# Kernel optimization log

Hardware: AMD Instinct MI355X
Metric: run time of the kernel (lower is better)

The kernel has to match this reference:

```python
import jax, jax.numpy as jnp
import numpy as np
import math

D_MODEL = 512
EXPAND = 1
D_INNER = EXPAND * D_MODEL          # 512
HALF = D_INNER // 2                 # 256 per-branch channels
D_STATE = D_MODEL // 4 * EXPAND     # 128 (overrides d_state arg in __init__)
DT_RANK = math.ceil(D_MODEL / 16)   # 32
D_CONV = 4


def _dwconv_same(x, w):
    # x: (B, C, L), w: (C, 1, k); torch padding='same' for k=4 -> pad (left=1, right=2)
    k = w.shape[-1]
    total = k - 1
    left = total // 2
    return jax.lax.conv_general_dilated(
        x, w, window_strides=(1,), padding=[(left, total - left)],
        feature_group_count=w.shape[0], dimension_numbers=("NCH", "OIH", "NCH"))


def _sparse_approx(m):
    thr = jnp.max(m) * 0.1
    return jnp.sign(m) * jax.nn.relu(jnp.abs(m) - thr)


def _selective_scan(u, delta, A, Bc, Cc, D):
    # u, delta: (B, d, L); A: (d, n); Bc, Cc: (B, n, L); D: (d,)
    dT = jnp.moveaxis(delta, 2, 0)   # (L, B, d)
    uT = jnp.moveaxis(u, 2, 0)       # (L, B, d)
    BT = jnp.moveaxis(Bc, 2, 0)      # (L, B, n)
    CT = jnp.moveaxis(Cc, 2, 0)      # (L, B, n)

    def step(h, inputs):
        d_t, u_t, b_t, c_t = inputs                      # (B,d),(B,d),(B,n),(B,n)
        dA = jnp.exp(d_t[..., None] * A)                 # (B, d, n)
        dBu = d_t[..., None] * b_t[:, None, :] * u_t[..., None]
        h = dA * h + dBu                                 # (B, d, n)
        y = jnp.einsum("bdn,bn->bd", h, c_t)
        return h, y

    h0 = jnp.zeros((u.shape[0], u.shape[1], A.shape[1]), dtype=u.dtype)
    _, ys = jax.lax.scan(step, h0, (dT, uT, BT, CT))     # ys: (L, B, d)
    y = jnp.moveaxis(ys, 0, 2)                           # (B, d, L)
    return y + u * D[:, None]


def _branch(inph, in_w, cx_w, cz_w, xproj_w, dt_w, dt_b, out_w, A, D):
    # inph: (B, L, d_model)
    xz = jnp.swapaxes(inph @ in_w.T, 1, 2)   # (B, d_inner, L)
    x, z = xz[:, :HALF], xz[:, HALF:]
    x = jax.nn.silu(_dwconv_same(x, cx_w))   # (B, half, L); conv bias is False (True//2==0)
    z = jax.nn.silu(_dwconv_same(z, cz_w))
    x_dbl = jnp.swapaxes(x, 1, 2) @ xproj_w.T        # (B, L, dt_rank + 2n)
    dt = x_dbl[..., :DT_RANK] @ dt_w.T               # (B, L, half)
    dt = jnp.swapaxes(dt, 1, 2)                      # (B, half, L)
    Bc = jnp.swapaxes(x_dbl[..., DT_RANK:DT_RANK + D_STATE], 1, 2)   # (B, n, L)
    Cc = jnp.swapaxes(x_dbl[..., DT_RANK + D_STATE:], 1, 2)          # (B, n, L)
    Bc = _sparse_approx(Bc)
    Cc = _sparse_approx(Cc)
    delta = jax.nn.softplus(dt + dt_b[None, :, None])
    y = _selective_scan(x, delta, A, Bc, Cc, D)
    out = jnp.concatenate([y, z], axis=1)            # (B, d_inner, L)
    return jnp.swapaxes(out, 1, 2) @ out_w.T         # (B, L, d_model)


def setup_inputs() -> dict:
    key = jax.random.key(0)
    ks = jax.random.split(key, 16)
    B, L = 2, 2048
    s = lambda fan: 1.0 / np.sqrt(fan)

    inp = jax.random.normal(ks[0], (B, 2 * D_MODEL, L), jnp.float32)

    in_proj_w = jax.random.uniform(ks[1], (D_INNER, D_MODEL), jnp.float32, -s(D_MODEL), s(D_MODEL))
    x_proj_w = jax.random.uniform(ks[2], (DT_RANK + 2 * D_STATE, HALF), jnp.float32, -s(HALF), s(HALF))
    dt_init_std = DT_RANK ** (-0.5)
    dt_proj_w = jax.random.uniform(ks[3], (HALF, DT_RANK), jnp.float32, -dt_init_std, dt_init_std)
    out_proj_w = jax.random.uniform(ks[4], (D_MODEL, D_INNER), jnp.float32, -s(D_INNER), s(D_INNER))

    in_proj_2_w = jax.random.uniform(ks[5], (D_INNER, D_MODEL), jnp.float32, -s(D_MODEL), s(D_MODEL))
    x_proj_2_w = jax.random.uniform(ks[6], (DT_RANK + 2 * D_STATE, HALF), jnp.float32, -s(HALF), s(HALF))
    dt_proj_2_w = jax.random.uniform(ks[7], (HALF, DT_RANK), jnp.float32, -dt_init_std, dt_init_std)
    out_proj_2_w = jax.random.uniform(ks[8], (D_MODEL, D_INNER), jnp.float32, -s(D_INNER), s(D_INNER))

    # dt bias init: inverse-softplus of dt ~ LogUniform(1e-3, 1e-1), floor 1e-4
    def inv_softplus_dt(k):
        u = jax.random.uniform(k, (HALF,), jnp.float32)
        dt = jnp.exp(u * (np.log(0.1) - np.log(0.001)) + np.log(0.001))
        dt = jnp.clip(dt, 1e-4, None)
        return dt + jnp.log(-jnp.expm1(-dt))
    dt_proj_b = inv_softplus_dt(ks[9])
    dt_proj_2_b = inv_softplus_dt(ks[10])

    cs = 1.0 / np.sqrt(D_CONV)  # depthwise conv fan_in = 1*k
    conv_x_w = jax.random.uniform(ks[11], (HALF, 1, D_CONV), jnp.float32, -cs, cs)
    conv_z_w = jax.random.uniform(ks[12], (HALF, 1, D_CONV), jnp.float32, -cs, cs)
    conv_x_2_w = jax.random.uniform(ks[13], (HALF, 1, D_CONV), jnp.float32, -cs, cs)
    conv_z_2_w = jax.random.uniform(ks[14], (HALF, 1, D_CONV), jnp.float32, -cs, cs)

    A_log = jnp.log(jnp.broadcast_to(jnp.arange(1, D_STATE + 1, dtype=jnp.float32), (HALF, D_STATE)))
    D = jnp.ones((HALF,), jnp.float32)
    epsilon = jnp.array([0.01], jnp.float32)

    return dict(inp=inp, in_proj_w=in_proj_w, conv_x_w=conv_x_w, conv_z_w=conv_z_w,
                x_proj_w=x_proj_w, dt_proj_w=dt_proj_w, dt_proj_b=dt_proj_b, out_proj_w=out_proj_w,
                in_proj_2_w=in_proj_2_w, conv_x_2_w=conv_x_2_w, conv_z_2_w=conv_z_2_w,
                x_proj_2_w=x_proj_2_w, dt_proj_2_w=dt_proj_2_w, dt_proj_2_b=dt_proj_2_b,
                out_proj_2_w=out_proj_2_w, A_log=A_log, D=D, epsilon=epsilon)


def reference(inp, in_proj_w, conv_x_w, conv_z_w, x_proj_w, dt_proj_w, dt_proj_b, out_proj_w,
              in_proj_2_w, conv_x_2_w, conv_z_2_w, x_proj_2_w, dt_proj_2_w, dt_proj_2_b,
              out_proj_2_w, A_log, D, epsilon):
    # inp: (B, 2*d_model, L) -> split along dim 1, permute to (B, L, d_model)
    inpx = jnp.swapaxes(inp[:, :D_MODEL, :], 1, 2)
    inpy = jnp.swapaxes(inp[:, D_MODEL:, :], 1, 2)

    A_base = (1.0 + epsilon[0]) * (-jnp.exp(A_log))
    A1 = _sparse_approx(A_base)        # branch 1
    A2 = _sparse_approx(A1)            # branch 2 sparsifies the already-sparsified A

    out1 = _branch(inpx, in_proj_w, conv_x_w, conv_z_w, x_proj_w, dt_proj_w, dt_proj_b, out_proj_w, A1, D)
    out2 = _branch(inpy, in_proj_2_w, conv_x_2_w, conv_z_2_w, x_proj_2_w, dt_proj_2_w, dt_proj_2_b, out_proj_2_w, A2, D)
    return out1, out2
```

## Files before the change

kernel.cpp:

```cpp
#include <hip/hip_runtime.h>
#include <math.h>

constexpr int B_    = 2;
constexpr int L_    = 2048;
constexpr int NROW  = B_ * L_;
constexpr int MROW  = 2 * NROW;
constexpr int HALF_ = 256;
constexpr int DS_   = 128;

constexpr float LOG2E = 1.4426950408889634f;

constexpr size_t OFF_MINP = 0;
constexpr size_t OFF_BCMX = 32;
constexpr size_t OFF_XZ   = 64;
constexpr size_t OFF_YT   = OFF_XZ + (size_t)MROW * 256;
constexpr size_t OFF_XDBL = OFF_XZ + (size_t)MROW * 512;
constexpr size_t OFF_XS   = OFF_XDBL + (size_t)MROW * 288;
constexpr size_t OFF_BS   = OFF_XS  + (size_t)MROW * 256;
constexpr size_t OFF_CS   = OFF_BS  + (size_t)2 * NROW * 128;
constexpr size_t OFF_DTT  = OFF_CS  + (size_t)2 * NROW * 128;
constexpr size_t OFF_DUT  = OFF_DTT + (size_t)2 * 256 * 4096;
constexpr size_t OFF_UDT  = OFF_DUT + (size_t)2 * 256 * 4096;
constexpr size_t FLOAT_END = OFF_UDT + (size_t)2 * 256 * 4096;

constexpr size_t HOFF_XINH = 0;
constexpr size_t HOFF_XINL = HOFF_XINH + (size_t)MROW * 512;
constexpr size_t HOFF_YZH  = HOFF_XINH;
constexpr size_t HOFF_YZL  = HOFF_XINL;
constexpr size_t HOFF_XSH  = HOFF_XINL + (size_t)MROW * 512;
constexpr size_t HOFF_XSL  = HOFF_XSH  + (size_t)MROW * 256;
constexpr size_t HOFF_INWH = HOFF_XSL  + (size_t)MROW * 256;
constexpr size_t HOFF_INWL = HOFF_INWH + 524288;
constexpr size_t HOFF_XWH  = HOFF_INWL + 524288;
constexpr size_t HOFF_XWL  = HOFF_XWH  + 147456;
constexpr size_t HOFF_OUTWH= HOFF_XWL  + 147456;
constexpr size_t HOFF_OUTWL= HOFF_OUTWH+ 524288;

constexpr size_t WST_IN = 262144;
constexpr size_t WST_X  = 73728;

constexpr int PRE_MINA = 32;
constexpr int PRE_WSPL = (1196032 + 255) / 256;
constexpr int PRE_TIN  = 64 * 16 * 4;
constexpr int PRE_BLOCKS = PRE_MINA + PRE_WSPL + PRE_TIN;

typedef __bf16 bf16x8 __attribute__((ext_vector_type(8)));
typedef float  f32x4  __attribute__((ext_vector_type(4)));

__device__ __forceinline__ unsigned short bf16rn(float x) {
    unsigned u = __float_as_uint(x);
    unsigned r = (u + 0x7FFFu + ((u >> 16) & 1u)) >> 16;
    return (unsigned short)r;
}
__device__ __forceinline__ void split2(float x, unsigned short& h, unsigned short& l) {
    h = bf16rn(x);
    float hf = __uint_as_float(((unsigned)h) << 16);
    l = bf16rn(x - hf);
}

__device__ __forceinline__ float shrinkf(float v, float thr) {
    float a = fabsf(v) - thr;
    a = fmaxf(a, 0.0f);
    float r = copysignf(a, v);
    return (v == 0.0f) ? 0.0f : r;
}
__device__ __forceinline__ float siluf(float v) { return v / (1.0f + __expf(-v)); }
__device__ __forceinline__ float softplusf(float v) {
    return fmaxf(v, 0.0f) + log1pf(__expf(-fabsf(v)));
}
__device__ __forceinline__ float rlanef(float v, int l) {
    return __int_as_float(__builtin_amdgcn_readlane(__float_as_int(v), l));
}
__device__ __forceinline__ unsigned fkey(float f) {
    unsigned u = __float_as_uint(f);
    return (u >> 31) ? ~u : (u | 0x80000000u);
}
__device__ __forceinline__ float funkey(unsigned k) {
    unsigned u = (k >> 31) ? (k & 0x7FFFFFFFu) : ~k;
    return __uint_as_float(u);
}

__global__ __launch_bounds__(256) void pre_all(const float* __restrict__ A_log,
                                               const float* __restrict__ inp,
                                               const float* __restrict__ in_w0,
                                               const float* __restrict__ in_w1,
                                               const float* __restrict__ outw0,
                                               const float* __restrict__ outw1,
                                               const float* __restrict__ xw0,
                                               const float* __restrict__ xw1,
                                               float* __restrict__ ws,
                                               unsigned* __restrict__ bcmax,
                                               unsigned short* __restrict__ hb) {
    int bid = blockIdx.x;
    int tid = threadIdx.x;
    if (bid < PRE_MINA) {
        __shared__ float sbuf[8];
        int i = bid * 1024 + tid * 4;
        float4 v = *(const float4*)(A_log + i);
        float mv = fminf(fminf(v.x, v.y), fminf(v.z, v.w));
        #pragma unroll
        for (int off = 32; off > 0; off >>= 1) mv = fminf(mv, __shfl_xor(mv, off));
        if ((tid & 63) == 0) sbuf[tid >> 6] = mv;
        __syncthreads();
        if (tid == 0) {
            float r = fminf(fminf(sbuf[0], sbuf[1]), fminf(sbuf[2], sbuf[3]));
            ws[OFF_MINP + bid] = r;
        }
        if (bid == 0 && tid < 4) bcmax[tid] = 0u;
    } else if (bid < PRE_MINA + PRE_WSPL) {
        int i = (bid - PRE_MINA) * 256 + tid;
        if (i >= 1196032) return;
        const float* src;
        size_t hbase, lbase;
        int off;
        if (i < 1048576) {
            int t = i >> 18;
            off = i & 262143;
            src = (t == 0) ? in_w0 : (t == 1) ? in_w1 : (t == 2) ? outw0 : outw1;
            if (t < 2) { hbase = HOFF_INWH + (size_t)t * WST_IN;  lbase = HOFF_INWL + (size_t)t * WST_IN; }
            else       { hbase = HOFF_OUTWH + (size_t)(t - 2) * WST_IN; lbase = HOFF_OUTWL + (size_t)(t - 2) * WST_IN; }
        } else {
            int j = i - 1048576;
            int t = (j < (int)WST_X) ? 0 : 1;
            off = j - t * (int)WST_X;
            src = t ? xw1 : xw0;
            hbase = HOFF_XWH + (size_t)t * WST_X;
            lbase = HOFF_XWL + (size_t)t * WST_X;
        }
        unsigned short h, l;
        split2(src[off], h, l);
        hb[hbase + off] = h;
        hb[lbase + off] = l;
    } else {
        __shared__ float tile[32][33];
        int idx = bid - PRE_MINA - PRE_WSPL;
        int bx = idx & 63;
        int by = (idx >> 6) & 15;
        int z  = idx >> 10;
        int br = z >> 1;
        int b  = z & 1;
        int t0 = bx * 32;
        int m0 = by * 32;
        int tx = tid & 31;
        int ty = tid >> 5;
        #pragma unroll
        for (int k = 0; k < 4; k++) {
            tile[ty + 8 * k][tx] =
                inp[((size_t)b * 1024 + br * 512 + m0 + ty + 8 * k) * L_ + t0 + tx];
        }
        __syncthreads();
        #pragma unroll
        for (int k = 0; k < 4; k++) {
            size_t dst = ((size_t)br * NROW + (size_t)b * L_ + t0 + ty + 8 * k) * 512 + m0 + tx;
            unsigned short h, l;
            split2(tile[tx][ty + 8 * k], h, l);
            hb[HOFF_XINH + dst] = h;
            hb[HOFF_XINL + dst] = l;
        }
    }
}

template <int NGUARD, int DOMAX>
__global__ __launch_bounds__(256) void gemm_mfma(const unsigned short* __restrict__ Ah,
                                                 const unsigned short* __restrict__ Al, int lda,
                                                 const unsigned short* __restrict__ WhB,
                                                 const unsigned short* __restrict__ WlB,
                                                 size_t wstride,
                                                 float* __restrict__ C, int ldc,
                                                 int N, int K,
                                                 unsigned* __restrict__ bcmax) {
    __shared__ __align__(16) unsigned short sAh[128 * 40];
    __shared__ __align__(16) unsigned short sAl[128 * 40];
    __shared__ __align__(16) unsigned short sBh[64 * 40];
    __shared__ __align__(16) unsigned short sBl[64 * 40];
    int tid  = threadIdx.x;
    int wid  = tid >> 6;
    int lane = tid & 63;
    int fr   = lane & 15;
    int kg   = lane >> 4;
    int mblk = blockIdx.y * 128;
    int nblk = blockIdx.x * 64;
    int br   = (mblk >= NROW) ? 1 : 0;
    const unsigned short* Wh = WhB + (size_t)br * wstride;
    const unsigned short* Wl = WlB + (size_t)br * wstride;
    int srow = tid >> 2;
    int skp  = (tid & 3) * 8;
    bool brow_ok = (!NGUARD) || ((nblk + srow) < N);

    const unsigned short* pA0 = Ah + (size_t)(mblk + srow) * lda + skp;
    const unsigned short* pA1 = Ah + (size_t)(mblk + 64 + srow) * lda + skp;
    const unsigned short* pL0 = Al + (size_t)(mblk + srow) * lda + skp;
    const unsigned short* pL1 = Al + (size_t)(mblk + 64 + srow) * lda + skp;
    const unsigned short* pBh = Wh + (size_t)(nblk + srow) * K + skp;
    const unsigned short* pBl = Wl + (size_t)(nblk + srow) * K + skp;

    f32x4 acc[2][4] = {};

    uint4 rah0 = *(const uint4*)(pA0);
    uint4 rah1 = *(const uint4*)(pA1);
    uint4 ral0 = *(const uint4*)(pL0);
    uint4 ral1 = *(const uint4*)(pL1);
    uint4 rbh = {0, 0, 0, 0}, rbl = {0, 0, 0, 0};
    if (brow_ok) {
        rbh = *(const uint4*)(pBh);
        rbl = *(const uint4*)(pBl);
    }

    for (int k0 = 0; k0 < K; k0 += 32) {
        __syncthreads();
        *(uint4*)(sAh + srow * 40 + skp) = rah0;
        *(uint4*)(sAh + (64 + srow) * 40 + skp) = rah1;
        *(uint4*)(sAl + srow * 40 + skp) = ral0;
        *(uint4*)(sAl + (64 + srow) * 40 + skp) = ral1;
        *(uint4*)(sBh + srow * 40 + skp) = rbh;
        *(uint4*)(sBl + srow * 40 + skp) = rbl;
        __syncthreads();

        int kn = k0 + 32;
        if (kn < K) {
            rah0 = *(const uint4*)(pA0 + kn);
            rah1 = *(const uint4*)(pA1 + kn);
            ral0 = *(const uint4*)(pL0 + kn);
            ral1 = *(const uint4*)(pL1 + kn);
            if (brow_ok) {
                rbh = *(const uint4*)(pBh + kn);
                rbl = *(const uint4*)(pBl + kn);
            }
        }

        bf16x8 ah0 = *(const bf16x8*)(sAh + (wid * 32 + fr) * 40 + kg * 8);
        bf16x8 ah1 = *(const bf16x8*)(sAh + (wid * 32 + 16 + fr) * 40 + kg * 8);
        bf16x8 al0 = *(const bf16x8*)(sAl + (wid * 32 + fr) * 40 + kg * 8);
        bf16x8 al1 = *(const bf16x8*)(sAl + (wid * 32 + 16 + fr) * 40 + kg * 8);
        #pragma unroll
        for (int nt = 0; nt < 4; nt++) {
            bf16x8 bh = *(const bf16x8*)(sBh + (nt * 16 + fr) * 40 + kg * 8);
            bf16x8 bl = *(const bf16x8*)(sBl + (nt * 16 + fr) * 40 + kg * 8);
            acc[0][nt] = __builtin_amdgcn_mfma_f32_16x16x32_bf16(ah0, bh, acc[0][nt], 0, 0, 0);
            acc[0][nt] = __builtin_amdgcn_mfma_f32_16x16x32_bf16(ah0, bl, acc[0][nt], 0, 0, 0);
            acc[0][nt] = __builtin_amdgcn_mfma_f32_16x16x32_bf16(al0, bh, acc[0][nt], 0, 0, 0);
            acc[1][nt] = __builtin_amdgcn_mfma_f32_16x16x32_bf16(ah1, bh, acc[1][nt], 0, 0, 0);
            acc[1][nt] = __builtin_amdgcn_mfma_f32_16x16x32_bf16(ah1, bl, acc[1][nt], 0, 0, 0);
            acc[1][nt] = __builtin_amdgcn_mfma_f32_16x16x32_bf16(al1, bh, acc[1][nt], 0, 0, 0);
        }
    }
    #pragma unroll
    for (int mt = 0; mt < 2; mt++) {
        #pragma unroll
        for (int nt = 0; nt < 4; nt++) {
            int col = nblk + nt * 16 + fr;
            if (NGUARD && col >= N) continue;
            #pragma unroll
            for (int r = 0; r < 4; r++) {
                int row = mblk + wid * 32 + mt * 16 + kg * 4 + r;
                C[(size_t)row * ldc + col] = acc[mt][nt][r];
            }
        }
    }
    if (DOMAX) {
        float mb = -INFINITY, mc = -INFINITY;
        #pragma unroll
        for (int nt = 0; nt < 4; nt++) {
            int c16 = nblk + nt * 16;
            if (c16 >= 32 && c16 < 160) {
                #pragma unroll
                for (int mt = 0; mt < 2; mt++)
                    #pragma unroll
                    for (int r = 0; r < 4; r++) mb = fmaxf(mb, acc[mt][nt][r]);
            } else if (c16 >= 160 && c16 < 288) {
                #pragma unroll
                for (int mt = 0; mt < 2; mt++)
                    #pragma unroll
                    for (int r = 0; r < 4; r++) mc = fmaxf(mc, acc[mt][nt][r]);
            }
        }
        #pragma unroll
        for (int off = 32; off > 0; off >>= 1) {
            mb = fmaxf(mb, __shfl_xor(mb, off));
            mc = fmaxf(mc, __shfl_xor(mc, off));
        }
        if (lane == 0) {
            if (mb > -INFINITY) atomicMax(bcmax + 2 * br,     fkey(mb));
            if (mc > -INFINITY) atomicMax(bcmax + 2 * br + 1, fkey(mc));
        }
    }
}

__global__ __launch_bounds__(256) void conv_silu_kernel(const float* __restrict__ xz,
                                                        float* __restrict__ xs,
                                                        unsigned short* __restrict__ xsh,
                                                        unsigned short* __restrict__ xsl,
                                                        unsigned short* __restrict__ yzh,
                                                        unsigned short* __restrict__ yzl,
                                                        const float* __restrict__ wx0,
                                                        const float* __restrict__ wx1,
                                                        const float* __restrict__ wz0,
                                                        const float* __restrict__ wz1) {
    int gid = blockIdx.x * 256 + threadIdx.x;
    int c4  = (gid & 63) << 2;
    int row = gid >> 6;
    int br  = row >> 12;
    int t   = row & (L_ - 1);
    const float* wx = br ? wx1 : wx0;
    const float* wz = br ? wz1 : wz0;
    float4 wxv[4], wzv[4];
    #pragma unroll
    for (int k = 0; k < 4; k++) {
        wxv[k] = *(const float4*)(wx + (c4 + k) * 4);
        wzv[k] = *(const float4*)(wz + (c4 + k) * 4);
    }
    float4 ax = {0, 0, 0, 0}, az = {0, 0, 0, 0};
    #pragma unroll
    for (int j = 0; j < 4; j++) {
        int tt = t + j - 1;
        if (tt >= 0 && tt < L_) {
            const float* p = xz + (size_t)(row + j - 1) * 512;
            float4 vx = *(const float4*)(p + c4);
            float4 vz = *(const float4*)(p + 256 + c4);
            ax.x = fmaf(vx.x, ((const float*)&wxv[0])[j], ax.x);
            ax.y = fmaf(vx.y, ((const float*)&wxv[1])[j], ax.y);
            ax.z = fmaf(vx.z, ((const float*)&wxv[2])[j], ax.z);
            ax.w = fmaf(vx.w, ((const float*)&wxv[3])[j], ax.w);
            az.x = fmaf(vz.x, ((const float*)&wzv[0])[j], az.x);
            az.y = fmaf(vz.y, ((const float*)&wzv[1])[j], az.y);
            az.z = fmaf(vz.z, ((const float*)&wzv[2])[j], az.z);
            az.w = fmaf(vz.w, ((const float*)&wzv[3])[j], az.w);
        }
    }
    float4 sx, sz;
    sx.x = siluf(ax.x); sx.y = siluf(ax.y); sx.z = siluf(ax.z); sx.w = siluf(ax.w);
    sz.x = siluf(az.x); sz.y = siluf(az.y); sz.z = siluf(az.z); sz.w = siluf(az.w);
    *(float4*)(xs + (size_t)row * 256 + c4) = sx;
    ushort4 hx, lx, hz, lz;
    split2(sx.x, hx.x, lx.x); split2(sx.y, hx.y, lx.y);
    split2(sx.z, hx.z, lx.z); split2(sx.w, hx.w, lx.w);
    split2(sz.x, hz.x, lz.x); split2(sz.y, hz.y, lz.y);
    split2(sz.z, hz.z, lz.z); split2(sz.w, hz.w, lz.w);
    *(ushort4*)(xsh + (size_t)row * 256 + c4) = hx;
    *(ushort4*)(xsl + (size_t)row * 256 + c4) = lx;
    *(ushort4*)(yzh + (size_t)row * 512 + 256 + c4) = hz;
    *(ushort4*)(yzl + (size_t)row * 512 + 256 + c4) = lz;
}

__global__ __launch_bounds__(256) void dtprep_shrink(const float* __restrict__ A, int lda,
                                                     const float* __restrict__ W0,
                                                     const float* __restrict__ W1,
                                                     const float* __restrict__ b0,
                                                     const float* __restrict__ b1,
                                                     const float* __restrict__ xs,
                                                     const float* __restrict__ Dvec,
                                                     float* __restrict__ dtT,
                                                     float* __restrict__ duT,
                                                     float* __restrict__ udT,
                                                     const unsigned* __restrict__ bcmax,
                                                     float* __restrict__ Bs,
                                                     float* __restrict__ Cs) {
    __shared__ float As[16][68];
    __shared__ float Ws[16][68];
    __shared__ float tb[64 * 68];
    int tid = threadIdx.x;
    int kk = tid & 15;
    int rr = tid >> 4;
    int mblk = blockIdx.y * 64;
    int nblk = blockIdx.x * 64;
    int br = (mblk >= NROW) ? 1 : 0;
    const float* W    = br ? W1 : W0;
    const float* bias = br ? b1 : b0;
    float acc[4][4] = {};
    for (int k0 = 0; k0 < 32; k0 += 16) {
        #pragma unroll
        for (int j = 0; j < 4; j++) {
            As[kk][rr + 16 * j] = A[(size_t)(mblk + rr + 16 * j) * lda + k0 + kk];
        }
        #pragma unroll
        for (int j = 0; j < 4; j++) {
            Ws[kk][rr + 16 * j] = W[(size_t)(nblk + rr + 16 * j) * 32 + k0 + kk];
        }
        __syncthreads();
        int ty = tid >> 4;
        int tx = tid & 15;
        #pragma unroll
        for (int kq = 0; kq < 16; kq++) {
            float a0 = As[kq][ty * 4 + 0];
            float a1 = As[kq][ty * 4 + 1];
            float a2 = As[kq][ty * 4 + 2];
            float a3 = As[kq][ty * 4 + 3];
            float v0 = Ws[kq][tx * 4 + 0];
            float v1 = Ws[kq][tx * 4 + 1];
            float v2 = Ws[kq][tx * 4 + 2];
            float v3 = Ws[kq][tx * 4 + 3];
            acc[0][0] = fmaf(a0, v0, acc[0][0]); acc[0][1] = fmaf(a0, v1, acc[0][1]);
            acc[0][2] = fmaf(a0, v2, acc[0][2]); acc[0][3] = fmaf(a0, v3, acc[0][3]);
            acc[1][0] = fmaf(a1, v0, acc[1][0]); acc[1][1] = fmaf(a1, v1, acc[1][1]);
            acc[1][2] = fmaf(a1, v2, acc[1][2]); acc[1][3] = fmaf(a1, v3, acc[1][3]);
            acc[2][0] = fmaf(a2, v0, acc[2][0]); acc[2][1] = fmaf(a2, v1, acc[2][1]);
            acc[2][2] = fmaf(a2, v2, acc[2][2]); acc[2][3] = fmaf(a2, v3, acc[2][3]);
            acc[3][0] = fmaf(a3, v0, acc[3][0]); acc[3][1] = fmaf(a3, v1, acc[3][1]);
            acc[3][2] = fmaf(a3, v2, acc[3][2]); acc[3][3] = fmaf(a3, v3, acc[3][3]);
        }
        __syncthreads();
    }
    int ty = tid >> 4;
    int tx = tid & 15;
    float dlt[4][4], uu[4][4];
    #pragma unroll
    for (int i = 0; i < 4; i++) {
        int m = mblk + ty * 4 + i;
        #pragma unroll
        for (int j = 0; j < 4; j++) {
            int n = nblk + tx * 4 + j;
            dlt[i][j] = softplusf(acc[i][j] + bias[n]);
            uu[i][j]  = xs[(size_t)m * 256 + n];
        }
    }
    float Dv[4];
    #pragma unroll
    for (int j = 0; j < 4; j++) Dv[j] = Dvec[nblk + tx * 4 + j];

    int mlocbase = mblk & (NROW - 1);
    int nrd  = tid >> 2;
    int mc   = (tid & 3) * 4;
    size_t obase = ((size_t)br * 256 + nblk + nrd) * 4096 + mlocbase;
    #pragma unroll
    for (int pass = 0; pass < 3; pass++) {
        __syncthreads();
        #pragma unroll
        for (int i = 0; i < 4; i++) {
            #pragma unroll
            for (int j = 0; j < 4; j++) {
                float v = (pass == 0) ? dlt[i][j] * LOG2E
                        : (pass == 1) ? dlt[i][j] * uu[i][j]
                                      : uu[i][j] * Dv[j];
                tb[(tx * 4 + j) * 68 + ty * 4 + i] = v;
            }
        }
        __syncthreads();
        float* dst = (pass == 0) ? dtT : (pass == 1) ? duT : udT;
        #pragma unroll
        for (int it = 0; it < 4; it++) {
            int cc = mc + it * 16;
            float4 v = *(const float4*)(tb + nrd * 68 + cc);
            *(float4*)(dst + obase + cc) = v;
        }
    }
    {
        int q = blockIdx.x;
        int isC = q >> 1;
        int cbase = (q & 1) * 64;
        int xoff = isC ? (160 + cbase) : (32 + cbase);
        float thr = 0.1f * funkey(bcmax[2 * br + isC]);
        float* dstArr = isC ? Cs : Bs;
        int r = tid >> 2;
        int c0 = (tid & 3) * 16;
        const float* src = A + (size_t)(mblk + r) * lda + xoff + c0;
        float* dp = dstArr + (size_t)(mblk + r) * 128 + cbase + c0;
        #pragma unroll
        for (int i = 0; i < 16; i += 4) {
            float4 v = *(const float4*)(src + i);
            float4 o;
            o.x = shrinkf(v.x, thr);
            o.y = shrinkf(v.y, thr);
            o.z = shrinkf(v.z, thr);
            o.w = shrinkf(v.w, thr);
            *(float4*)(dp + i) = o;
        }
    }
}

__global__ __launch_bounds__(128) void scan10_kernel(float* __restrict__ ws,
                                                     const float* __restrict__ A_log,
                                                     const float* __restrict__ eps) {
    int blk  = blockIdx.x;
    int xcd  = blk & 7;
    int slot = blk >> 3;
    int combo = xcd >> 1;
    int d  = (xcd & 1) * 128 + slot;
    int br = combo >> 1;
    int b  = combo & 1;
    int tid = threadIdx.x;
    int lt  = tid & 63;
    int half = tid >> 6;

    float pv = ws[OFF_MINP + (tid & 31)];
    #pragma unroll
    for (int off = 16; off > 0; off >>= 1) pv = fminf(pv, __shfl_xor(pv, off));
    float e  = 1.0f + eps[0];
    float m1 = -e * __expf(pv);
    float t1 = 0.1f * m1;
    float t2 = 0.1f * shrinkf(m1, t1);
    float base = -e * __expf(A_log[d * 128 + tid]);
    float a = shrinkf(base, t1);
    if (br) a = shrinkf(a, t2);

    size_t dchain = ((size_t)br * 256 + d) * 4096 + (size_t)b * L_;
    const float* dtp = ws + OFF_DTT + dchain;
    const float* dup = ws + OFF_DUT + dchain;
    const float* udp = ws + OFF_UDT + dchain;
    const float* Bq  = ws + OFF_BS + ((size_t)br * NROW + (size_t)b * L_) * 128 + tid;
    const float* Cq  = ws + OFF_CS + ((size_t)br * NROW + (size_t)b * L_) * 128 + tid;
    float*       yTp = ws + OFF_YT + dchain;

    __shared__ float red[64 * 132];
    __shared__ float comb[2][64];

    float h = 0.0f;

    float Bb[2][8], Cb[2][8];
    #pragma unroll
    for (int j = 0; j < 8; j++) { Bb[0][j] = Bq[j * 128]; Cb[0][j] = Cq[j * 128]; }
    Bq += 1024; Cq += 1024;
    #pragma unroll
    for (int j = 0; j < 8; j++) { Bb[1][j] = Bq[j * 128]; Cb[1][j] = Cq[j * 128]; }
    Bq += 1024; Cq += 1024;

    float dt_c = dtp[lt];
    float du_c = dup[lt];
    float dt_n = 0.0f, du_n = 0.0f;

    for (int c = 0; c < 32; c++) {
        if (c < 31) { dt_n = dtp[64 + lt]; du_n = dup[64 + lt]; }
        dtp += 64; dup += 64;
        float ud_c = udp[c * 64 + lt];
        #pragma unroll
        for (int m = 0; m < 8; m++) {
            const int cur = m & 1;
            #pragma unroll
            for (int j = 0; j < 8; j++) {
                const int tl = m * 8 + j;
                float dt2 = rlanef(dt_c, tl);
                float du  = rlanef(du_c, tl);
                float ev = __builtin_amdgcn_exp2f(dt2 * a);
                h = fmaf(ev, h, du * Bb[cur][j]);
                red[tl * 132 + half * 64 + lt] = h * Cb[cur][j];
            }
            #pragma unroll
            for (int j = 0; j < 8; j++) {
                Bb[cur][j] = Bq[j * 128];
                Cb[cur][j] = Cq[j * 128];
            }
            Bq += 1024; Cq += 1024;
        }
        __builtin_amdgcn_wave_barrier();
        {
            const float* rp = &red[lt * 132 + half * 64];
            float s0 = 0.f, s1 = 0.f, s2 = 0.f, s3 = 0.f;
            #pragma unroll
            for (int i = 0; i < 64; i += 4) {
                float4 v = *(const float4*)(rp + i);
                s0 += v.x; s1 += v.y; s2 += v.z; s3 += v.w;
            }
            float part = (s0 + s1) + (s2 + s3);
            if (half) comb[c & 1][lt] = part;
            __syncthreads();
            if (!half) yTp[c * 64 + lt] = part + comb[c & 1][lt] + ud_c;
        }
        __builtin_amdgcn_wave_barrier();
        dt_c = dt_n;
        du_c = du_n;
    }
}

__global__ __launch_bounds__(256) void transpose_yz_kernel(const float* __restrict__ yT,
                                                           unsigned short* __restrict__ yzh,
                                                           unsigned short* __restrict__ yzl) {
    __shared__ float tile[32][33];
    int br = blockIdx.z;
    int m0 = blockIdx.x * 32;
    int n0 = blockIdx.y * 32;
    int tx = threadIdx.x;
    int ty = threadIdx.y;
    #pragma unroll
    for (int k = 0; k < 4; k++) {
        tile[ty + 8 * k][tx] = yT[((size_t)br * 256 + m0 + ty + 8 * k) * 4096 + n0 + tx];
    }
    __syncthreads();
    #pragma unroll
    for (int k = 0; k < 4; k++) {
        size_t dst = ((size_t)br * NROW + n0 + ty + 8 * k) * 512 + m0 + tx;
        unsigned short h, l;
        split2(tile[tx][ty + 8 * k], h, l);
        yzh[dst] = h; yzl[dst] = l;
    }
}

extern "C" void kernel_launch(void* const* d_in, const int* in_sizes, int n_in,
                              void* d_out, int out_size, void* d_ws, size_t ws_size,
                              hipStream_t stream) {
    const float* inp   = (const float*)d_in[0];
    const float* in_w[2]  = {(const float*)d_in[1],  (const float*)d_in[8]};
    const float* cxw[2]   = {(const float*)d_in[2],  (const float*)d_in[9]};
    const float* czw[2]   = {(const float*)d_in[3],  (const float*)d_in[10]};
    const float* xw[2]    = {(const float*)d_in[4],  (const float*)d_in[11]};
    const float* dtw[2]   = {(const float*)d_in[5],  (const float*)d_in[12]};
    const float* dtb[2]   = {(const float*)d_in[6],  (const float*)d_in[13]};
    const float* outw[2]  = {(const float*)d_in[7],  (const float*)d_in[14]};
    const float* A_log = (const float*)d_in[15];
    const float* Dvec  = (const float*)d_in[16];
    const float* eps   = (const float*)d_in[17];
    float* out = (float*)d_out;
    float* ws  = (float*)d_ws;
    unsigned short* hb = (unsigned short*)(ws + FLOAT_END);
    unsigned* bcmax = (unsigned*)(ws + OFF_BCMX);

    pre_all<<<PRE_BLOCKS, 256, 0, stream>>>(
        A_log, inp, in_w[0], in_w[1], outw[0], outw[1], xw[0], xw[1],
        ws, bcmax, hb);

    gemm_mfma<0, 0><<<dim3(512 / 64, MROW / 128), 256, 0, stream>>>(
        hb + HOFF_XINH, hb + HOFF_XINL, 512,
        hb + HOFF_INWH, hb + HOFF_INWL, WST_IN,
        ws + OFF_XZ, 512, 512, 512, nullptr);

    conv_silu_kernel<<<(MROW * 64) / 256, 256, 0, stream>>>(
        ws + OFF_XZ, ws + OFF_XS, hb + HOFF_XSH, hb + HOFF_XSL,
        hb + HOFF_YZH, hb + HOFF_YZL, cxw[0], cxw[1], czw[0], czw[1]);

    gemm_mfma<1, 1><<<dim3((288 + 63) / 64, MROW / 128), 256, 0, stream>>>(
        hb + HOFF_XSH, hb + HOFF_XSL, 256,
        hb + HOFF_XWH, hb + HOFF_XWL, WST_X,
        ws + OFF_XDBL, 288, 288, 256, bcmax);

    dtprep_shrink<<<dim3(4, MROW / 64), 256, 0, stream>>>(
        ws + OFF_XDBL, 288, dtw[0], dtw[1], dtb[0], dtb[1],
        ws + OFF_XS, Dvec,
        ws + OFF_DTT, ws + OFF_DUT, ws + OFF_UDT,
        bcmax, ws + OFF_BS, ws + OFF_CS);

    scan10_kernel<<<dim3(1024), 128, 0, stream>>>(ws, A_log, eps);

    transpose_yz_kernel<<<dim3(256 / 32, NROW / 32, 2), dim3(32, 8), 0, stream>>>(
        ws + OFF_YT, hb + HOFF_YZH, hb + HOFF_YZL);

    gemm_mfma<0, 0><<<dim3(512 / 64, MROW / 128), 256, 0, stream>>>(
        hb + HOFF_YZH, hb + HOFF_YZL, 512,
        hb + HOFF_OUTWH, hb + HOFF_OUTWL, WST_IN,
        out, 512, 512, 512, nullptr);
}
```

Baseline: 322.3 us.

## Split selective scan into two-pass chunked scan over sequence halves

The single sequential scan over 2048 timesteps is replaced by two kernels. The first runs the state recurrence over the first half only, without the C reduction, and stores the final hidden state. The second processes both sequence halves in parallel, seeding the second half with the stored state. This shortens the serial dependency chain and raises parallelism, in exchange for recomputing the first half's recurrence and an extra kernel launch.

```diff
diff --git a/kernel.cpp b/kernel.cpp
--- a/kernel.cpp
+++ b/kernel.cpp
@@ -13,6 +13,7 @@
 constexpr size_t OFF_MINP = 0;
 constexpr size_t OFF_BCMX = 32;
 constexpr size_t OFF_XZ   = 64;
+constexpr size_t OFF_HIN  = OFF_XZ;
 constexpr size_t OFF_YT   = OFF_XZ + (size_t)MROW * 256;
 constexpr size_t OFF_XDBL = OFF_XZ + (size_t)MROW * 512;
 constexpr size_t OFF_XS   = OFF_XDBL + (size_t)MROW * 288;
@@ -467,9 +468,9 @@
     }
 }
 
-__global__ __launch_bounds__(128) void scan10_kernel(float* __restrict__ ws,
-                                                     const float* __restrict__ A_log,
-                                                     const float* __restrict__ eps) {
+__global__ __launch_bounds__(128) void scan_pass1(float* __restrict__ ws,
+                                                  const float* __restrict__ A_log,
+                                                  const float* __restrict__ eps) {
     int blk  = blockIdx.x;
     int xcd  = blk & 7;
     int slot = blk >> 3;
@@ -479,7 +480,6 @@
     int b  = combo & 1;
     int tid = threadIdx.x;
     int lt  = tid & 63;
-    int half = tid >> 6;
 
     float pv = ws[OFF_MINP + (tid & 31)];
     #pragma unroll
@@ -495,32 +495,26 @@
     size_t dchain = ((size_t)br * 256 + d) * 4096 + (size_t)b * L_;
     const float* dtp = ws + OFF_DTT + dchain;
     const float* dup = ws + OFF_DUT + dchain;
-    const float* udp = ws + OFF_UDT + dchain;
     const float* Bq  = ws + OFF_BS + ((size_t)br * NROW + (size_t)b * L_) * 128 + tid;
     const float* Cq  = ws + OFF_CS + ((size_t)br * NROW + (size_t)b * L_) * 128 + tid;
-    float*       yTp = ws + OFF_YT + dchain;
-
-    __shared__ float red[64 * 132];
-    __shared__ float comb[2][64];
+    (void)Cq;
 
     float h = 0.0f;
-
-    float Bb[2][8], Cb[2][8];
-    #pragma unroll
-    for (int j = 0; j < 8; j++) { Bb[0][j] = Bq[j * 128]; Cb[0][j] = Cq[j * 128]; }
-    Bq += 1024; Cq += 1024;
-    #pragma unroll
-    for (int j = 0; j < 8; j++) { Bb[1][j] = Bq[j * 128]; Cb[1][j] = Cq[j * 128]; }
-    Bq += 1024; Cq += 1024;
+    float Bb[2][8];
+    #pragma unroll
+    for (int j = 0; j < 8; j++) Bb[0][j] = Bq[j * 128];
+    Bq += 1024;
+    #pragma unroll
+    for (int j = 0; j < 8; j++) Bb[1][j] = Bq[j * 128];
+    Bq += 1024;
 
     float dt_c = dtp[lt];
     float du_c = dup[lt];
     float dt_n = 0.0f, du_n = 0.0f;
 
-    for (int c = 0; c < 32; c++) {
-        if (c < 31) { dt_n = dtp[64 + lt]; du_n = dup[64 + lt]; }
+    for (int c = 0; c < 16; c++) {
+        if (c < 15) { dt_n = dtp[64 + lt]; du_n = dup[64 + lt]; }
         dtp += 64; dup += 64;
-        float ud_c = udp[c * 64 + lt];
         #pragma unroll
         for (int m = 0; m < 8; m++) {
             const int cur = m & 1;
@@ -531,30 +525,122 @@
                 float du  = rlanef(du_c, tl);
                 float ev = __builtin_amdgcn_exp2f(dt2 * a);
                 h = fmaf(ev, h, du * Bb[cur][j]);
-                red[tl * 132 + half * 64 + lt] = h * Cb[cur][j];
             }
             #pragma unroll
-            for (int j = 0; j < 8; j++) {
-                Bb[cur][j] = Bq[j * 128];
-                Cb[cur][j] = Cq[j * 128];
+            for (int j = 0; j < 8; j++) Bb[cur][j] = Bq[j * 128];
+            Bq += 1024;
+        }
+        dt_c = dt_n;
+        du_c = du_n;
+    }
+    ws[OFF_HIN + (((size_t)(br * 2 + b) * 256 + d) * 128 + tid)] = h;
+}
+
+__global__ __launch_bounds__(256) void scan_pass2(float* __restrict__ ws,
+                                                  const float* __restrict__ A_log,
+                                                  const float* __restrict__ eps) {
+    int blk  = blockIdx.x;
+    int xcd  = blk & 7;
+    int slot = blk >> 3;
+    int dhalf = xcd & 1;
+    int combo = xcd >> 1;
+    int br = combo >> 1;
+    int b  = combo & 1;
+    int chunk = slot >> 6;
+    int pairIdx = slot & 63;
+    int tid = threadIdx.x;
+    int ch  = tid >> 7;
+    int nid = tid & 127;
+    int lt  = tid & 63;
+    int half = (tid >> 6) & 1;
+    int d = dhalf * 128 + pairIdx * 2 + ch;
+
+    float pv = ws[OFF_MINP + (tid & 31)];
+    #pragma unroll
+    for (int off = 16; off > 0; off >>= 1) pv = fminf(pv, __shfl_xor(pv, off));
+    float e  = 1.0f + eps[0];
+    float m1 = -e * __expf(pv);
+    float t1 = 0.1f * m1;
+    float t2 = 0.1f * shrinkf(m1, t1);
+    float base = -e * __expf(A_log[d * 128 + nid]);
+    float a = shrinkf(base, t1);
+    if (br) a = shrinkf(a, t2);
+
+    size_t dchain = ((size_t)br * 256 + d) * 4096 + (size_t)b * L_;
+    size_t tb0 = (size_t)chunk * 1024;
+    const float* dtp = ws + OFF_DTT + dchain + tb0;
+    const float* dup = ws + OFF_DUT + dchain + tb0;
+    const float* udp = ws + OFF_UDT + dchain + tb0;
+    const float* Bq  = ws + OFF_BS + ((size_t)br * NROW + (size_t)b * L_ + tb0) * 128 + nid;
+    const float* Cq  = ws + OFF_CS + ((size_t)br * NROW + (size_t)b * L_ + tb0) * 128 + nid;
+    float*       yTp = ws + OFF_YT + dchain + tb0;
+
+    __shared__ float red[2][32 * 132];
+    __shared__ float comb[2][2][32];
+
+    float h = 0.0f;
+    if (chunk) h = ws[OFF_HIN + (((size_t)(br * 2 + b) * 256 + d) * 128 + nid)];
+
+    float Bb[2][8], Cb[2][8];
+    #pragma unroll
+    for (int j = 0; j < 8; j++) { Bb[0][j] = Bq[j * 128]; Cb[0][j] = Cq[j * 128]; }
+    Bq += 1024; Cq += 1024;
+    #pragma unroll
+    for (int j = 0; j < 8; j++) { Bb[1][j] = Bq[j * 128]; Cb[1][j] = Cq[j * 128]; }
+    Bq += 1024; Cq += 1024;
+
+    float dt_c = dtp[lt];
+    float du_c = dup[lt];
+    float dt_n = 0.0f, du_n = 0.0f;
+
+    int tp = lt >> 1;
+    int q  = lt & 1;
+
+    for (int cc = 0; cc < 16; cc++) {
+        if (cc < 15) { dt_n = dtp[64 + lt]; du_n = dup[64 + lt]; }
+        dtp += 64; dup += 64;
+        #pragma unroll
+        for (int g = 0; g < 2; g++) {
+            float ud_c = udp[cc * 64 + g * 32 + tp];
+            #pragma unroll
+            for (int m = 0; m < 4; m++) {
+                const int cur = m & 1;
+                #pragma unroll
+                for (int j = 0; j < 8; j++) {
+                    const int tl = g * 32 + m * 8 + j;
+                    const int tloc = m * 8 + j;
+                    float dt2 = rlanef(dt_c, tl);
+                    float du  = rlanef(du_c, tl);
+                    float ev = __builtin_amdgcn_exp2f(dt2 * a);
+                    h = fmaf(ev, h, du * Bb[cur][j]);
+                    red[ch][tloc * 132 + half * 64 + lt] = h * Cb[cur][j];
+                }
+                #pragma unroll
+                for (int j = 0; j < 8; j++) {
+                    Bb[cur][j] = Bq[j * 128];
+                    Cb[cur][j] = Cq[j * 128];
+                }
+                Bq += 1024; Cq += 1024;
             }
-            Bq += 1024; Cq += 1024;
-        }
-        __builtin_amdgcn_wave_barrier();
-        {
-            const float* rp = &red[lt * 132 + half * 64];
-            float s0 = 0.f, s1 = 0.f, s2 = 0.f, s3 = 0.f;
-            #pragma unroll
-            for (int i = 0; i < 64; i += 4) {
-                float4 v = *(const float4*)(rp + i);
-                s0 += v.x; s1 += v.y; s2 += v.z; s3 += v.w;
+            __builtin_amdgcn_wave_barrier();
+            {
+                const float* rp = &red[ch][tp * 132 + half * 64 + q * 32];
+                float s0 = 0.f, s1 = 0.f, s2 = 0.f, s3 = 0.f;
+                #pragma unroll
+                for (int i = 0; i < 32; i += 4) {
+                    float4 v = *(const float4*)(rp + i);
+                    s0 += v.x; s1 += v.y; s2 += v.z; s3 += v.w;
+                }
+                float part = (s0 + s1) + (s2 + s3);
+                float tot = part + __shfl_xor(part, 1);
+                int par = (cc * 2 + g) & 1;
+                if (half) comb[ch][par][tp] = tot;
+                __syncthreads();
+                if (half == 0 && q == 0)
+                    yTp[cc * 64 + g * 32 + tp] = tot + comb[ch][par][tp] + ud_c;
             }
-            float part = (s0 + s1) + (s2 + s3);
-            if (half) comb[c & 1][lt] = part;
-            __syncthreads();
-            if (!half) yTp[c * 64 + lt] = part + comb[c & 1][lt] + ud_c;
-        }
-        __builtin_amdgcn_wave_barrier();
+            __builtin_amdgcn_wave_barrier();
+        }
         dt_c = dt_n;
         du_c = du_n;
     }
@@ -626,7 +712,8 @@
         ws + OFF_DTT, ws + OFF_DUT, ws + OFF_UDT,
         bcmax, ws + OFF_BS, ws + OFF_CS);
 
-    scan10_kernel<<<dim3(1024), 128, 0, stream>>>(ws, A_log, eps);
+    scan_pass1<<<dim3(1024), 128, 0, stream>>>(ws, A_log, eps);
+    scan_pass2<<<dim3(1024), 256, 0, stream>>>(ws, A_log, eps);
 
     transpose_yz_kernel<<<dim3(256 / 32, NROW / 32, 2), dim3(32, 8), 0, stream>>>(
         ws + OFF_YT, hb + HOFF_YZH, hb + HOFF_YZL);
```

New measurement: 350.2 us. +8.7%, slower.
